# Kernel optimization log

Measured on AMD Instinct MI355X. Metric: run time of the kernel, lower is better.

The kernel has to match this reference:

```python
import jax, jax.numpy as jnp
import numpy as np

N, D, V = 4096, 512, 100000


def setup_inputs() -> dict:
    key = jax.random.key(0)
    k1, k2, k3 = jax.random.split(key, 3)
    x = jax.random.normal(k1, (N, D), dtype=jnp.float32)
    lb = jax.random.randint(k2, (N,), 0, V, dtype=jnp.int64)
    W = jax.random.normal(k3, (V, D), dtype=jnp.float32) * 0.02
    b = jnp.zeros((V,), dtype=jnp.float32)
    return {"x": x, "lb": lb, "W": W, "b": b}


def reference(x, lb, W, b):
    # fc: logits[N, V] = x @ W^T + b
    logits = jnp.einsum('nd,vd->nv', x, W) + b
    # numerically-stable softmax cross-entropy, mean reduction
    logz = jax.nn.logsumexp(logits, axis=-1)               # [N]
    tgt = jnp.take_along_axis(logits, lb[:, None], axis=-1)[:, 0]  # [N]
    loss = jnp.mean(logz - tgt)
    return loss
```

## Files before the change

### kernel.cpp

```cpp
#include <hip/hip_runtime.h>
#include <hip/hip_bf16.h>
#include <math.h>


#define N_ROWS 4096
#define DIM    512
#define VOCAB  100000
#define NTILES 782
#define VPAD   (NTILES * 128)
#define SPLITS 32
#define TPS    25
#define XELEMS (N_ROWS * DIM)
#define WVALID ((size_t)VOCAB * DIM)
#define WBYTES ((size_t)VPAD * DIM)
#define TILEB  (128 * DIM)

#define LOG2E 1.44269504088896340736f

typedef __attribute__((ext_vector_type(4))) int   i32x4;
typedef __attribute__((ext_vector_type(8))) int   i32x8;
typedef __attribute__((ext_vector_type(4))) float f32x4;

#define WAITV0() asm volatile("s_waitcnt vmcnt(0)" ::: "memory")
#define BARRIER_PIN()                         \
  do {                                        \
    __builtin_amdgcn_s_barrier();             \
    __builtin_amdgcn_sched_barrier(0);        \
  } while (0)


__device__ __forceinline__ void gload_lds16(const char* g, char* l) {
  __builtin_amdgcn_global_load_lds(
      (const __attribute__((address_space(1))) unsigned int*)g,
      (__attribute__((address_space(3))) unsigned int*)l, 16, 0, 0);
}

__device__ __forceinline__ int pack4_fp8(float4 f, float sc) {
  int p = __builtin_amdgcn_cvt_pk_fp8_f32(f.x * sc, f.y * sc, 0, false);
  p = __builtin_amdgcn_cvt_pk_fp8_f32(f.z * sc, f.w * sc, p, true);
  return p;
}

__device__ __forceinline__ i32x8 frag32(const char* base) {
  i32x4 lo = *(const i32x4*)(base);
  i32x4 hi = *(const i32x4*)(base + 1024);
  return (i32x8){lo.x, lo.y, lo.z, lo.w, hi.x, hi.y, hi.z, hi.w};
}


__global__ __launch_bounds__(256) void cvt_kernel(const float* __restrict__ x,
                                                  const float* __restrict__ W,
                                                  char* __restrict__ out8) {
  const size_t e = ((size_t)blockIdx.x * 256 + threadIdx.x) * 16;
  int4 o;
  if (e < (size_t)XELEMS) {
    const float4* s = (const float4*)(x + e);
    o.x = pack4_fp8(s[0], LOG2E); o.y = pack4_fp8(s[1], LOG2E);
    o.z = pack4_fp8(s[2], LOG2E); o.w = pack4_fp8(s[3], LOG2E);
  } else if (e - XELEMS < WVALID) {
    const float4* s = (const float4*)(W + (e - XELEMS));
    o.x = pack4_fp8(s[0], 32.f); o.y = pack4_fp8(s[1], 32.f);
    o.z = pack4_fp8(s[2], 32.f); o.w = pack4_fp8(s[3], 32.f);
  } else {
    o.x = 0; o.y = 0; o.z = 0; o.w = 0;
  }
  *(int4*)(out8 + e) = o;
}


__global__ __launch_bounds__(256) void tgt_kernel(const float* __restrict__ x,
                                                  const int* __restrict__ lb,
                                                  const float* __restrict__ W,
                                                  const float* __restrict__ bias,
                                                  float* __restrict__ tgt) {
  const int wv = threadIdx.x >> 6;
  const int lane = threadIdx.x & 63;
  const int row = blockIdx.x * 4 + wv;
  const int t = lb[row];
  const float* xr = x + (size_t)row * DIM;
  const float* wr = W + (size_t)t * DIM;
  float s = 0.f;
#pragma unroll
  for (int i = 0; i < 8; ++i) s += xr[lane + i * 64] * wr[lane + i * 64];
#pragma unroll
  for (int m = 32; m; m >>= 1) s += __shfl_xor(s, m);
  if (lane == 0) tgt[row] = s + bias[t];
}


__global__ __launch_bounds__(256, 2) void lse_kernel(const char* __restrict__ xb,
                                                     const char* __restrict__ wb,
                                                     const float* __restrict__ bias,
                                                     float* __restrict__ spart) {
  __shared__ __align__(16) char ldsB[2][32768];
  __shared__ float ldsBias[TPS * 128];

  const int d = blockIdx.x;
  const int s     = 2 * (d & 7) + ((d >> 3) & 1) + 16 * (d >> 9);
  const int mtile = (d >> 4) & 31;

  const int m0 = mtile * 128;
  const int t0 = s * TPS;
  const int t1 = (t0 + TPS < NTILES) ? (t0 + TPS) : NTILES;
  const int NT = t1 - t0;

  const int tid  = threadIdx.x;
  const int lane = tid & 63;
  const int wv   = tid >> 6;
  const int rh   = wv >> 1;
  const int ch   = wv & 1;
  const int fr   = lane & 15;
  const int fq   = lane >> 4;

  i32x8 Aa[4][4];
  {
    const char* ax = xb + (size_t)(m0 + 64 * rh + fr) * DIM + fq * 32;
#pragma unroll
    for (int rf = 0; rf < 4; ++rf)
#pragma unroll
      for (int ks = 0; ks < 4; ++ks) {
        const char* p = ax + rf * (16 * DIM) + ks * 128;
        i32x4 lo = *(const i32x4*)p;
        i32x4 hi = *(const i32x4*)(p + 16);
        Aa[rf][ks] = (i32x8){lo.x, lo.y, lo.z, lo.w, hi.x, hi.y, hi.z, hi.w};
      }
  }

  for (int c = tid; c < NT * 128; c += 256) {
    const int col = t0 * 128 + c;
    ldsBias[c] = (col < VOCAB) ? bias[col] * LOG2E : -INFINITY;
  }
  __syncthreads();

  auto stagePhase = [&](const char* tileSrc, int kp, char* buf) {
#pragma unroll
    for (int ks2 = 0; ks2 < 2; ++ks2) {
      const char* s0 = tileSrc + (2 * kp + ks2) * 128 + fq * 32;
#pragma unroll
      for (int gg = 0; gg < 2; ++gg) {
        const int g = 2 * wv + gg;
        const char* src = s0 + (size_t)(16 * g + fr) * DIM;
        char* dst = buf + ks2 * 16384 + g * 2048;
        gload_lds16(src,      dst);
        gload_lds16(src + 16, dst + 1024);
      }
    }
  };

  float S[4][4];
#pragma unroll
  for (int rf = 0; rf < 4; ++rf)
#pragma unroll
    for (int r = 0; r < 4; ++r) S[rf][r] = 0.f;

  f32x4 acc[4][4];

#define COMPUTE_PHASE(bufR, ksA, ksB, FIRSTF)                               \
  {                                                                         \
    __builtin_amdgcn_s_setprio(1);                                          \
    _Pragma("unroll")                                                       \
    for (int c = 0; c < 4; ++c) {                                           \
      const char* fb = (bufR) + (4 * ch + c) * 2048 + lane * 16;            \
      const i32x8 bf0 = frag32(fb);                                         \
      const i32x8 bf1 = frag32(fb + 16384);                                 \
      _Pragma("unroll")                                                     \
      for (int rf = 0; rf < 4; ++rf) {                                      \
        acc[rf][c] = __builtin_amdgcn_mfma_scale_f32_16x16x128_f8f6f4(      \
            Aa[rf][ksA], bf0,                                               \
            (FIRSTF) ? (f32x4){0.f, 0.f, 0.f, 0.f} : acc[rf][c],            \
            0, 0, 0, 127, 0, 122);                                          \
        acc[rf][c] = __builtin_amdgcn_mfma_scale_f32_16x16x128_f8f6f4(      \
            Aa[rf][ksB], bf1, acc[rf][c], 0, 0, 0, 127, 0, 122);            \
      }                                                                     \
    }                                                                       \
    __builtin_amdgcn_s_setprio(0);                                          \
  }

  auto epilogue = [&](int ti) {
    const float* bT = &ldsBias[ti * 128 + 64 * ch];
    float badd[4];
#pragma unroll
    for (int c = 0; c < 4; ++c) badd[c] = bT[16 * c + fr];
#pragma unroll
    for (int rf = 0; rf < 4; ++rf)
#pragma unroll
      for (int r = 0; r < 4; ++r) {
        float sum = 0.f;
#pragma unroll
        for (int c = 0; c < 4; ++c)
          sum += __builtin_amdgcn_exp2f(acc[rf][c][r] + badd[c]);
        S[rf][r] += sum;
      }
  };

  const char* wt = wb + (size_t)t0 * TILEB;
  stagePhase(wt, 0, ldsB[0]);

  for (int tt = t0; tt < t1; ++tt, wt += TILEB) {
    WAITV0(); BARRIER_PIN();
    stagePhase(wt, 1, ldsB[1]);
    __builtin_amdgcn_sched_barrier(0);
    COMPUTE_PHASE(ldsB[0], 0, 1, true)

    WAITV0(); BARRIER_PIN();
    if (tt + 1 < t1) stagePhase(wt + TILEB, 0, ldsB[0]);
    __builtin_amdgcn_sched_barrier(0);
    COMPUTE_PHASE(ldsB[1], 2, 3, false)

    epilogue(tt - t0);
  }

  __syncthreads();
  float* sc = (float*)ldsB;
  if (ch == 1) {
    float* base = sc + (size_t)(rh * 64 + lane) * 20;
#pragma unroll
    for (int rf = 0; rf < 4; ++rf)
      *(float4*)(base + rf * 4) = (float4){S[rf][0], S[rf][1], S[rf][2], S[rf][3]};
  }
  __syncthreads();
  if (ch == 0) {
    const float* base = sc + (size_t)(rh * 64 + lane) * 20;
#pragma unroll
    for (int rf = 0; rf < 4; ++rf) {
      const float4 v = *(const float4*)(base + rf * 4);
      S[rf][0] += v.x; S[rf][1] += v.y; S[rf][2] += v.z; S[rf][3] += v.w;
    }
#pragma unroll
    for (int rf = 0; rf < 4; ++rf)
#pragma unroll
      for (int r = 0; r < 4; ++r) {
        float v = S[rf][r];
        v += __shfl_xor(v, 1);
        v += __shfl_xor(v, 2);
        v += __shfl_xor(v, 4);
        v += __shfl_xor(v, 8);
        if (fr == 0) {
          const int row = m0 + 64 * rh + 16 * rf + 4 * fq + r;
          spart[(size_t)row * SPLITS + s] = v;
        }
      }
  }
#undef COMPUTE_PHASE
}


__global__ __launch_bounds__(256) void combine_kernel(const float* __restrict__ spart,
                                                      const float* __restrict__ tgt,
                                                      float* __restrict__ out) {
  __shared__ float red[256];
  float local = 0.f;
  for (int r = threadIdx.x; r < N_ROWS; r += 256) {
    const float4* sp = (const float4*)(spart + (size_t)r * SPLITS);
    float st = 0.f;
#pragma unroll
    for (int i = 0; i < 8; ++i) { float4 v = sp[i]; st += (v.x + v.y) + (v.z + v.w); }
    local += __logf(st) - tgt[r];
  }
  red[threadIdx.x] = local;
  __syncthreads();
  for (int step = 128; step; step >>= 1) {
    if (threadIdx.x < step) red[threadIdx.x] += red[threadIdx.x + step];
    __syncthreads();
  }
  if (threadIdx.x == 0) out[0] = red[0] * (1.0f / (float)N_ROWS);
}


extern "C" void kernel_launch(void* const* d_in, const int* in_sizes, int n_in,
                              void* d_out, int out_size, void* d_ws, size_t ws_size,
                              hipStream_t stream) {
  const float* x  = (const float*)d_in[0];
  const int*   lb = (const int*)d_in[1];
  const float* W  = (const float*)d_in[2];
  const float* b  = (const float*)d_in[3];
  float* out = (float*)d_out;

  char* ws = (char*)d_ws;
  const size_t OFF_W   = (size_t)XELEMS;
  const size_t OFF_SP  = OFF_W + WBYTES;
  const size_t OFF_TGT = OFF_SP + (size_t)N_ROWS * SPLITS * 4;
  char*  xb    = ws;
  char*  wb    = ws + OFF_W;
  float* spart = (float*)(ws + OFF_SP);
  float* tgt   = (float*)(ws + OFF_TGT);

  cvt_kernel<<<13024, 256, 0, stream>>>(x, W, ws);
  tgt_kernel<<<1024, 256, 0, stream>>>(x, lb, W, b, tgt);
  lse_kernel<<<1024, 256, 0, stream>>>(xb, wb, b, spart);
  combine_kernel<<<1, 256, 0, stream>>>(spart, tgt, out);
}
```

Before: 557.8 us.

## Give each wave private LDS B buffers with per-k-step pipelining; fuse prep kernels

The LSE GEMM loop no longer stages a shared B tile with block-wide barriers. Each wave now streams its own 64 columns into a private double buffer, one k-slice at a time, and uses vmcnt-based waits so the next slice's loads overlap the MFMAs of the current one. This removes the s_barrier stalls, but waves in the same column half now load the same W data separately, which doubles LDS-fill traffic from L2. Separately, the fp8 conversion and target-logit kernels are merged into one launch, which saves one kernel launch and lets the two run concurrently.

```diff
diff --git a/kernel.cpp b/kernel.cpp
--- a/kernel.cpp
+++ b/kernel.cpp
@@ -14,19 +14,13 @@
 #define WVALID ((size_t)VOCAB * DIM)
 #define WBYTES ((size_t)VPAD * DIM)
 #define TILEB  (128 * DIM)
+#define CVT_BLOCKS 13024
 
 #define LOG2E 1.44269504088896340736f
 
 typedef __attribute__((ext_vector_type(4))) int   i32x4;
 typedef __attribute__((ext_vector_type(8))) int   i32x8;
 typedef __attribute__((ext_vector_type(4))) float f32x4;
-
-#define WAITV0() asm volatile("s_waitcnt vmcnt(0)" ::: "memory")
-#define BARRIER_PIN()                         \
-  do {                                        \
-    __builtin_amdgcn_s_barrier();             \
-    __builtin_amdgcn_sched_barrier(0);        \
-  } while (0)
 
 
 __device__ __forceinline__ void gload_lds16(const char* g, char* l) {
@@ -48,43 +42,41 @@
 }
 
 
-__global__ __launch_bounds__(256) void cvt_kernel(const float* __restrict__ x,
-                                                  const float* __restrict__ W,
-                                                  char* __restrict__ out8) {
-  const size_t e = ((size_t)blockIdx.x * 256 + threadIdx.x) * 16;
-  int4 o;
-  if (e < (size_t)XELEMS) {
-    const float4* s = (const float4*)(x + e);
-    o.x = pack4_fp8(s[0], LOG2E); o.y = pack4_fp8(s[1], LOG2E);
-    o.z = pack4_fp8(s[2], LOG2E); o.w = pack4_fp8(s[3], LOG2E);
-  } else if (e - XELEMS < WVALID) {
-    const float4* s = (const float4*)(W + (e - XELEMS));
-    o.x = pack4_fp8(s[0], 32.f); o.y = pack4_fp8(s[1], 32.f);
-    o.z = pack4_fp8(s[2], 32.f); o.w = pack4_fp8(s[3], 32.f);
+__global__ __launch_bounds__(256) void prep_kernel(const float* __restrict__ x,
+                                                   const float* __restrict__ W,
+                                                   char* __restrict__ out8,
+                                                   const int* __restrict__ lb,
+                                                   const float* __restrict__ bias,
+                                                   float* __restrict__ tgt) {
+  if (blockIdx.x < CVT_BLOCKS) {
+    const size_t e = ((size_t)blockIdx.x * 256 + threadIdx.x) * 16;
+    int4 o;
+    if (e < (size_t)XELEMS) {
+      const float4* s = (const float4*)(x + e);
+      o.x = pack4_fp8(s[0], LOG2E); o.y = pack4_fp8(s[1], LOG2E);
+      o.z = pack4_fp8(s[2], LOG2E); o.w = pack4_fp8(s[3], LOG2E);
+    } else if (e - XELEMS < WVALID) {
+      const float4* s = (const float4*)(W + (e - XELEMS));
+      o.x = pack4_fp8(s[0], 32.f); o.y = pack4_fp8(s[1], 32.f);
+      o.z = pack4_fp8(s[2], 32.f); o.w = pack4_fp8(s[3], 32.f);
+    } else {
+      o.x = 0; o.y = 0; o.z = 0; o.w = 0;
+    }
+    *(int4*)(out8 + e) = o;
   } else {
-    o.x = 0; o.y = 0; o.z = 0; o.w = 0;
-  }
-  *(int4*)(out8 + e) = o;
-}
-
-
-__global__ __launch_bounds__(256) void tgt_kernel(const float* __restrict__ x,
-                                                  const int* __restrict__ lb,
-                                                  const float* __restrict__ W,
-                                                  const float* __restrict__ bias,
-                                                  float* __restrict__ tgt) {
-  const int wv = threadIdx.x >> 6;
-  const int lane = threadIdx.x & 63;
-  const int row = blockIdx.x * 4 + wv;
-  const int t = lb[row];
-  const float* xr = x + (size_t)row * DIM;
-  const float* wr = W + (size_t)t * DIM;
-  float s = 0.f;
-#pragma unroll
-  for (int i = 0; i < 8; ++i) s += xr[lane + i * 64] * wr[lane + i * 64];
-#pragma unroll
-  for (int m = 32; m; m >>= 1) s += __shfl_xor(s, m);
-  if (lane == 0) tgt[row] = s + bias[t];
+    const int wv = threadIdx.x >> 6;
+    const int lane = threadIdx.x & 63;
+    const int row = (blockIdx.x - CVT_BLOCKS) * 4 + wv;
+    const int t = lb[row];
+    const float* xr = x + (size_t)row * DIM;
+    const float* wr = W + (size_t)t * DIM;
+    float s = 0.f;
+#pragma unroll
+    for (int i = 0; i < 8; ++i) s += xr[lane + i * 64] * wr[lane + i * 64];
+#pragma unroll
+    for (int m = 32; m; m >>= 1) s += __shfl_xor(s, m);
+    if (lane == 0) tgt[row] = s + bias[t];
+  }
 }
 
 
@@ -92,7 +84,7 @@
                                                      const char* __restrict__ wb,
                                                      const float* __restrict__ bias,
                                                      float* __restrict__ spart) {
-  __shared__ __align__(16) char ldsB[2][32768];
+  __shared__ __align__(16) char ldsB[4][2][8192];
   __shared__ float ldsBias[TPS * 128];
 
   const int d = blockIdx.x;
@@ -131,19 +123,20 @@
     ldsBias[c] = (col < VOCAB) ? bias[col] * LOG2E : -INFINITY;
   }
   __syncthreads();
-
-  auto stagePhase = [&](const char* tileSrc, int kp, char* buf) {
-#pragma unroll
-    for (int ks2 = 0; ks2 < 2; ++ks2) {
-      const char* s0 = tileSrc + (2 * kp + ks2) * 128 + fq * 32;
-#pragma unroll
-      for (int gg = 0; gg < 2; ++gg) {
-        const int g = 2 * wv + gg;
-        const char* src = s0 + (size_t)(16 * g + fr) * DIM;
-        char* dst = buf + ks2 * 16384 + g * 2048;
-        gload_lds16(src,      dst);
-        gload_lds16(src + 16, dst + 1024);
-      }
+  asm volatile("s_waitcnt vmcnt(0)" ::: "memory");
+  __builtin_amdgcn_sched_barrier(0);
+
+  char* const myB  = &ldsB[wv][0][0];
+  char* const buf0 = myB;
+  char* const buf1 = myB + 8192;
+  const size_t rowBase = (size_t)(64 * ch + fr) * DIM + fq * 32;
+
+  auto stageK = [&](const char* tileSrc, int ks, char* dst) {
+#pragma unroll
+    for (int gg = 0; gg < 4; ++gg) {
+      const char* src = tileSrc + rowBase + (size_t)(16 * gg) * DIM + ks * 128;
+      gload_lds16(src,      dst + gg * 2048);
+      gload_lds16(src + 16, dst + gg * 2048 + 1024);
     }
   };
 
@@ -155,25 +148,39 @@
 
   f32x4 acc[4][4];
 
-#define COMPUTE_PHASE(bufR, ksA, ksB, FIRSTF)                               \
-  {                                                                         \
-    __builtin_amdgcn_s_setprio(1);                                          \
-    _Pragma("unroll")                                                       \
-    for (int c = 0; c < 4; ++c) {                                           \
-      const char* fb = (bufR) + (4 * ch + c) * 2048 + lane * 16;            \
-      const i32x8 bf0 = frag32(fb);                                         \
-      const i32x8 bf1 = frag32(fb + 16384);                                 \
-      _Pragma("unroll")                                                     \
-      for (int rf = 0; rf < 4; ++rf) {                                      \
-        acc[rf][c] = __builtin_amdgcn_mfma_scale_f32_16x16x128_f8f6f4(      \
-            Aa[rf][ksA], bf0,                                               \
-            (FIRSTF) ? (f32x4){0.f, 0.f, 0.f, 0.f} : acc[rf][c],            \
-            0, 0, 0, 127, 0, 122);                                          \
-        acc[rf][c] = __builtin_amdgcn_mfma_scale_f32_16x16x128_f8f6f4(      \
-            Aa[rf][ksB], bf1, acc[rf][c], 0, 0, 0, 127, 0, 122);            \
-      }                                                                     \
-    }                                                                       \
-    __builtin_amdgcn_s_setprio(0);                                          \
+#define K_STEP(ksC, FIRSTF, WAITIMM, STAGE_EXPR)                              \
+  {                                                                           \
+    asm volatile("s_waitcnt vmcnt(" #WAITIMM ")" ::: "memory");               \
+    __builtin_amdgcn_sched_barrier(0);                                        \
+    const char* fb_ = myB + ((ksC) & 1) * 8192 + lane * 16;                   \
+    const i32x8 b0_ = frag32(fb_);                                            \
+    const i32x8 b1_ = frag32(fb_ + 2048);                                     \
+    const i32x8 b2_ = frag32(fb_ + 4096);                                     \
+    const i32x8 b3_ = frag32(fb_ + 6144);                                     \
+    asm volatile("s_waitcnt lgkmcnt(0)" ::: "memory");                        \
+    __builtin_amdgcn_sched_barrier(0);                                        \
+    STAGE_EXPR;                                                               \
+    __builtin_amdgcn_s_setprio(1);                                            \
+    _Pragma("unroll")                                                         \
+    for (int rf_ = 0; rf_ < 4; ++rf_) {                                       \
+      acc[rf_][0] = __builtin_amdgcn_mfma_scale_f32_16x16x128_f8f6f4(         \
+          Aa[rf_][ksC], b0_,                                                  \
+          (FIRSTF) ? (f32x4){0.f, 0.f, 0.f, 0.f} : acc[rf_][0],               \
+          0, 0, 0, 127, 0, 122);                                              \
+      acc[rf_][1] = __builtin_amdgcn_mfma_scale_f32_16x16x128_f8f6f4(         \
+          Aa[rf_][ksC], b1_,                                                  \
+          (FIRSTF) ? (f32x4){0.f, 0.f, 0.f, 0.f} : acc[rf_][1],               \
+          0, 0, 0, 127, 0, 122);                                              \
+      acc[rf_][2] = __builtin_amdgcn_mfma_scale_f32_16x16x128_f8f6f4(         \
+          Aa[rf_][ksC], b2_,                                                  \
+          (FIRSTF) ? (f32x4){0.f, 0.f, 0.f, 0.f} : acc[rf_][2],               \
+          0, 0, 0, 127, 0, 122);                                              \
+      acc[rf_][3] = __builtin_amdgcn_mfma_scale_f32_16x16x128_f8f6f4(         \
+          Aa[rf_][ksC], b3_,                                                  \
+          (FIRSTF) ? (f32x4){0.f, 0.f, 0.f, 0.f} : acc[rf_][3],               \
+          0, 0, 0, 127, 0, 122);                                              \
+    }                                                                         \
+    __builtin_amdgcn_s_setprio(0);                                            \
   }
 
   auto epilogue = [&](int ti) {
@@ -194,21 +201,26 @@
   };
 
   const char* wt = wb + (size_t)t0 * TILEB;
-  stagePhase(wt, 0, ldsB[0]);
-
-  for (int tt = t0; tt < t1; ++tt, wt += TILEB) {
-    WAITV0(); BARRIER_PIN();
-    stagePhase(wt, 1, ldsB[1]);
-    __builtin_amdgcn_sched_barrier(0);
-    COMPUTE_PHASE(ldsB[0], 0, 1, true)
-
-    WAITV0(); BARRIER_PIN();
-    if (tt + 1 < t1) stagePhase(wt + TILEB, 0, ldsB[0]);
-    __builtin_amdgcn_sched_barrier(0);
-    COMPUTE_PHASE(ldsB[1], 2, 3, false)
-
+
+  stageK(wt, 0, buf0);
+  stageK(wt, 1, buf1);
+
+  for (int tt = t0; tt < t1 - 1; ++tt, wt += TILEB) {
+    K_STEP(0, true,  8, stageK(wt, 2, buf0))
+    K_STEP(1, false, 8, stageK(wt, 3, buf1))
+    K_STEP(2, false, 8, stageK(wt + TILEB, 0, buf0))
+    K_STEP(3, false, 8, stageK(wt + TILEB, 1, buf1))
     epilogue(tt - t0);
   }
+
+  {
+    K_STEP(0, true,  8, stageK(wt, 2, buf0))
+    K_STEP(1, false, 8, stageK(wt, 3, buf1))
+    K_STEP(2, false, 8, (void)0)
+    K_STEP(3, false, 0, (void)0)
+    epilogue(NT - 1);
+  }
+#undef K_STEP
 
   __syncthreads();
   float* sc = (float*)ldsB;
@@ -241,7 +253,6 @@
         }
       }
   }
-#undef COMPUTE_PHASE
 }
 
 
@@ -285,8 +296,7 @@
   float* spart = (float*)(ws + OFF_SP);
   float* tgt   = (float*)(ws + OFF_TGT);
 
-  cvt_kernel<<<13024, 256, 0, stream>>>(x, W, ws);
-  tgt_kernel<<<1024, 256, 0, stream>>>(x, lb, W, b, tgt);
+  prep_kernel<<<CVT_BLOCKS + 1024, 256, 0, stream>>>(x, W, ws, lb, b, tgt);
   lse_kernel<<<1024, 256, 0, stream>>>(xb, wb, b, spart);
   combine_kernel<<<1, 256, 0, stream>>>(spart, tgt, out);
 }
```

New measurement: 780.0 us. 39.8% more time.
